# Kernel optimization log

Hardware: AMD Instinct MI355X
Metric: run time of the kernel (lower is better)

Reference implementation:

```python
import jax, jax.numpy as jnp
import numpy as np

N = 100000   # nodes
E = 1600000  # edges
G = 64       # graphs
D = 64       # latent_dim
NF = 128     # num_node_feats
EF = 32      # num_edge_feats
NV = 5000    # num_node_val_feats
LV = 3       # max_lv
EPS = 1e-5


def setup_inputs() -> dict:
    key = jax.random.key(0)
    ks = jax.random.split(key, 16)
    s = 0.05
    return {
        "node_feat": jax.random.normal(ks[0], (N, NF), jnp.float32),
        "edge_feat": jax.random.normal(ks[1], (E, EF), jnp.float32),
        "w_n2l_W": jax.random.normal(ks[2], (NF, D), jnp.float32) * s,
        "w_n2l_b": jnp.zeros((D,), jnp.float32),
        "node_val_embedding": jax.random.normal(ks[3], (NV, D), jnp.float32) * s,
        "w_e2l_W": jax.random.normal(ks[4], (LV + 1, EF, D), jnp.float32) * s,
        "w_e2l_b": jnp.zeros((LV + 1, D), jnp.float32),
        "conv_W": jax.random.normal(ks[5], (LV, D, D), jnp.float32) * s,
        "conv_b": jnp.zeros((LV, D), jnp.float32),
        "l2_W": jax.random.normal(ks[6], (LV, D, D), jnp.float32) * s,
        "l2_b": jnp.zeros((LV, D), jnp.float32),
        "msg_g": jnp.ones((LV + 1, D), jnp.float32),
        "msg_b": jnp.zeros((LV + 1, D), jnp.float32),
        "hid_g": jnp.ones((LV, D), jnp.float32),
        "hid_b": jnp.zeros((LV, D), jnp.float32),
        "out_W": jax.random.normal(ks[7], (D, D), jnp.float32) * s,
        "out_b": jnp.zeros((D,), jnp.float32),
        "edge_from": jax.random.randint(ks[8], (E,), 0, N, jnp.int32),
        "edge_to": jax.random.randint(ks[9], (E,), 0, N, jnp.int32),
        "g_idx": jnp.sort(jax.random.randint(ks[10], (N,), 0, G, jnp.int32)),
        "node_val_idx": jax.random.randint(ks[11], (N,), 0, NV, jnp.int32),
    }


def _bn(x, g, b):
    # BatchNorm1d in training mode: biased batch stats
    m = jnp.mean(x, axis=0)
    v = jnp.mean(jnp.square(x - m), axis=0)
    return (x - m) * jax.lax.rsqrt(v + EPS) * g + b


def reference(node_feat, edge_feat, w_n2l_W, w_n2l_b, node_val_embedding,
              w_e2l_W, w_e2l_b, conv_W, conv_b, l2_W, l2_b,
              msg_g, msg_b, hid_g, hid_b, out_W, out_b,
              edge_from, edge_to, g_idx, node_val_idx):
    act = jax.nn.relu
    # input node transform + sparse node-value embedding (one-hot spmm == gather)
    h = node_feat @ w_n2l_W + w_n2l_b + node_val_embedding[node_val_idx]
    # edge->node pool for level 0
    e0 = edge_feat @ w_e2l_W[0] + w_e2l_b[0]
    h = h + jax.ops.segment_sum(e0, edge_to, num_segments=N)
    h = _bn(act(h), msg_g[0], msg_b[0])
    for lv in range(LV):
        # MessagePassing with add-aggr: gather sources, scatter-add to targets, then Linear
        agg = jax.ops.segment_sum(h[edge_from], edge_to, num_segments=N)
        node_linear = agg @ conv_W[lv] + conv_b[lv]
        e = edge_feat @ w_e2l_W[lv + 1] + w_e2l_b[lv + 1]
        merged = act(node_linear + jax.ops.segment_sum(e, edge_to, num_segments=N))
        merged = _bn(merged, hid_g[lv], hid_b[lv])
        h = _bn(act(merged @ l2_W[lv] + l2_b[lv] + h), msg_g[lv + 1], msg_b[lv + 1])
    # readout: gnn_out='last', readout_agg='max', act_last=True, bn=False
    pooled = jax.ops.segment_max(h, g_idx, num_segments=G)
    return act(pooled @ out_W + out_b)
```

## Files before the change

kernel.cpp:

```cpp
#include <hip/hip_runtime.h>
#include <math.h>

#define NN 100000
#define EE 1600000
#define GG 64
#define DD 64
#define NF 128
#define EF 32
#define LVL 3
#define EPSBN 1e-5f
#define NTILES ((NN + 63) / 64)
#define NBS ((NN + 255) / 256)

typedef unsigned short u16;
typedef unsigned int u32;
typedef short s4v __attribute__((ext_vector_type(4)));
typedef short bf16x8 __attribute__((ext_vector_type(8)));
typedef float f32x4 __attribute__((ext_vector_type(4)));

__device__ __forceinline__ float4 ld4(const float* p) { return *(const float4*)p; }
__device__ __forceinline__ u16 f2b(float f) {
    u32 u = __float_as_uint(f);
    return (u16)((u + 0x7FFFu + ((u >> 16) & 1u)) >> 16);
}
__device__ __forceinline__ float b2f(u16 u) { return __uint_as_float(((u32)u) << 16); }
__device__ __forceinline__ float blo(u32 u) { return __uint_as_float(u << 16); }
__device__ __forceinline__ float bhi(u32 u) { return __uint_as_float(u & 0xFFFF0000u); }

__global__ void khist(const int* __restrict__ to, int* __restrict__ cnt) {
    int e = blockIdx.x * blockDim.x + threadIdx.x;
    if (e < EE) atomicAdd(&cnt[to[e]], 1);
}

__global__ void kbsum(const int* __restrict__ cnt, int* __restrict__ bsum) {
    __shared__ int s[256];
    int t = threadIdx.x;
    int i = blockIdx.x * 256 + t;
    s[t] = (i < NN) ? cnt[i] : 0;
    __syncthreads();
    for (int off = 128; off > 0; off >>= 1) {
        if (t < off) s[t] += s[t + off];
        __syncthreads();
    }
    if (t == 0) bsum[blockIdx.x] = s[0];
}

__global__ void kbscan(const int* __restrict__ bsum, int* __restrict__ boff) {
    __shared__ int s[512];
    int t = threadIdx.x;
    s[t] = (t < NBS) ? bsum[t] : 0;
    __syncthreads();
    for (int off = 1; off < 512; off <<= 1) {
        int v = (t >= off) ? s[t - off] : 0;
        __syncthreads();
        s[t] += v;
        __syncthreads();
    }
    if (t < NBS) boff[t] = (t == 0) ? 0 : s[t - 1];
}

__global__ void kfscan(const int* __restrict__ cnt, const int* __restrict__ boff,
                       int* __restrict__ row_ptr, int* __restrict__ cursor) {
    __shared__ int s[256];
    int t = threadIdx.x;
    int b = blockIdx.x;
    int i = b * 256 + t;
    int v = (i < NN) ? cnt[i] : 0;
    s[t] = v;
    __syncthreads();
    for (int off = 1; off < 256; off <<= 1) {
        int u = (t >= off) ? s[t - off] : 0;
        __syncthreads();
        s[t] += u;
        __syncthreads();
    }
    if (i < NN) {
        int excl = boff[b] + s[t] - v;
        row_ptr[i] = excl;
        cursor[i] = excl;
        if (i == NN - 1) row_ptr[NN] = boff[b] + s[t];
    }
}

__global__ void kreorder(const int* __restrict__ to, const int* __restrict__ from,
                         int* __restrict__ cursor, int2* __restrict__ pair) {
    int e = blockIdx.x * blockDim.x + threadIdx.x;
    if (e < EE) {
        int pos = atomicAdd(&cursor[to[e]], 1);
        pair[pos] = make_int2(e, from[e]);
    }
}

__global__ void kpool(const float* __restrict__ ef, const int* __restrict__ row_ptr,
                      const int2* __restrict__ pair, u16* __restrict__ pooled) {
    int lane = threadIdx.x & 63;
    int wid = threadIdx.x >> 6;
    int w = lane & 31, half = lane >> 5;
    for (int n = blockIdx.x * 4 + wid; n < NN; n += gridDim.x * 4) {
        int e0 = row_ptr[n], e1 = row_ptr[n + 1];
        float acc = 0.f;
        int e = e0 + half;
        for (; e + 2 < e1; e += 4) {
            int i0 = pair[e].x, i1 = pair[e + 2].x;
            float v0 = ef[(size_t)i0 * EF + w];
            float v1 = ef[(size_t)i1 * EF + w];
            acc += v0 + v1;
        }
        if (e < e1) acc += ef[(size_t)pair[e].x * EF + w];
        acc += __shfl_xor(acc, 32);
        if (half == 0) pooled[(size_t)n * EF + w] = f2b(acc);
    }
}

template <int K1, int K2, bool A1BF, bool AAFF, bool EMB, bool BE, bool RESID>
__global__ __launch_bounds__(256) void kgemm_mfma(
    const void* __restrict__ A1v, const u16* __restrict__ A2,
    const float* __restrict__ W1, const float* __restrict__ W2,
    const float* __restrict__ bias, const float* __restrict__ be,
    const int* __restrict__ row_ptr, const float* __restrict__ emb,
    const int* __restrict__ nvi, const u16* __restrict__ resid,
    const float* __restrict__ raff, const float* __restrict__ aaff,
    u16* __restrict__ Xb, float* __restrict__ stats) {
    constexpr int K = K1 + K2;
    constexpr int KP = K + 8;
    __shared__ u16 A_lds[64 * KP];
    __shared__ u16 Wt_lds[64 * KP];
    __shared__ float red[128];

    const int t = threadIdx.x;
    const int lane = t & 63;
    const int wv = t >> 6;
    const int l15 = lane & 15;
    const int lg = lane >> 4;

    for (int idx = t; idx < K * 16; idx += 256) {
        int k = idx >> 4, c4 = (idx & 15) * 4;
        float4 w4 = (k < K1) ? ld4(W1 + (size_t)k * 64 + c4)
                             : ld4(W2 + (size_t)(k - K1) * 64 + c4);
        Wt_lds[(c4 + 0) * KP + k] = f2b(w4.x);
        Wt_lds[(c4 + 1) * KP + k] = f2b(w4.y);
        Wt_lds[(c4 + 2) * KP + k] = f2b(w4.z);
        Wt_lds[(c4 + 3) * KP + k] = f2b(w4.w);
    }
    if (t < 128) red[t] = 0.f;

    float bias_c[4], be_c[4], rsc_c[4], rsh_c[4];
#pragma unroll
    for (int n = 0; n < 4; n++) {
        int ch = 16 * n + l15;
        bias_c[n] = bias[ch];
        be_c[n] = BE ? be[ch] : 0.f;
        rsc_c[n] = RESID ? raff[ch] : 0.f;
        rsh_c[n] = RESID ? raff[64 + ch] : 0.f;
    }

    for (int tile = blockIdx.x; tile < NTILES; tile += gridDim.x) {
        int nb = tile * 64;
        __syncthreads();
        if (A1BF) {
            const u16* A1b = (const u16*)A1v;
            for (int idx = t; idx < 64 * (K1 / 4); idx += 256) {
                int node = idx / (K1 / 4), kq = (idx % (K1 / 4)) * 4;
                int gn = nb + node;
                s4v v = {0, 0, 0, 0};
                if (gn < NN) {
                    v = *(const s4v*)(A1b + (size_t)gn * K1 + kq);
                    if (AAFF) {
#pragma unroll
                        for (int i = 0; i < 4; i++) {
                            float f = b2f((u16)v[i]) * aaff[kq + i] + aaff[64 + kq + i];
                            v[i] = (short)f2b(f);
                        }
                    }
                }
                *(s4v*)&A_lds[node * KP + kq] = v;
            }
        } else {
            const float* A1f = (const float*)A1v;
            for (int idx = t; idx < 64 * (K1 / 4); idx += 256) {
                int node = idx / (K1 / 4), kq = (idx % (K1 / 4)) * 4;
                int gn = nb + node;
                s4v v = {0, 0, 0, 0};
                if (gn < NN) {
                    float4 a = ld4(A1f + (size_t)gn * K1 + kq);
                    v[0] = (short)f2b(a.x); v[1] = (short)f2b(a.y);
                    v[2] = (short)f2b(a.z); v[3] = (short)f2b(a.w);
                }
                *(s4v*)&A_lds[node * KP + kq] = v;
            }
        }
        if (K2 > 0) {
            for (int idx = t; idx < 64 * (K2 / 4); idx += 256) {
                int node = idx / (K2 / 4), kq = (idx % (K2 / 4)) * 4;
                int gn = nb + node;
                s4v v = {0, 0, 0, 0};
                if (gn < NN) v = *(const s4v*)(A2 + (size_t)gn * K2 + kq);
                *(s4v*)&A_lds[node * KP + K1 + kq] = v;
            }
        }
        __syncthreads();

        f32x4 acc[4];
#pragma unroll
        for (int n = 0; n < 4; n++) acc[n] = (f32x4){0.f, 0.f, 0.f, 0.f};
        const int arow = 16 * wv + l15;
#pragma unroll
        for (int kk = 0; kk < K; kk += 32) {
            s4v alo = *(const s4v*)&A_lds[arow * KP + kk + lg * 4];
            s4v ahi = *(const s4v*)&A_lds[arow * KP + kk + lg * 4 + 16];
            bf16x8 a = __builtin_shufflevector(alo, ahi, 0, 1, 2, 3, 4, 5, 6, 7);
#pragma unroll
            for (int n = 0; n < 4; n++) {
                s4v wlo = *(const s4v*)&Wt_lds[(16 * n + l15) * KP + kk + lg * 4];
                s4v whi = *(const s4v*)&Wt_lds[(16 * n + l15) * KP + kk + lg * 4 + 16];
                bf16x8 b = __builtin_shufflevector(wlo, whi, 0, 1, 2, 3, 4, 5, 6, 7);
                acc[n] = __builtin_amdgcn_mfma_f32_16x16x32_bf16(a, b, acc[n], 0, 0, 0);
            }
        }

        float ss[4] = {0, 0, 0, 0}, sq2[4] = {0, 0, 0, 0};
#pragma unroll
        for (int r = 0; r < 4; r++) {
            int node = nb + 16 * wv + lg * 4 + r;
            if (node < NN) {
                float deg = BE ? (float)(row_ptr[node + 1] - row_ptr[node]) : 0.f;
                int nv = EMB ? nvi[node] : 0;
#pragma unroll
                for (int n = 0; n < 4; n++) {
                    int ch = 16 * n + l15;
                    float v = acc[n][r] + bias_c[n];
                    if (BE) v += deg * be_c[n];
                    if (EMB) v += emb[(size_t)nv * 64 + ch];
                    if (RESID) v += b2f(resid[(size_t)node * 64 + ch]) * rsc_c[n] + rsh_c[n];
                    v = fmaxf(v, 0.f);
                    Xb[(size_t)node * 64 + ch] = f2b(v);
                    ss[n] += v;
                    sq2[n] += v * v;
                }
            }
        }
#pragma unroll
        for (int n = 0; n < 4; n++) {
            float a = ss[n];
            a += __shfl_xor(a, 16);
            a += __shfl_xor(a, 32);
            float b = sq2[n];
            b += __shfl_xor(b, 16);
            b += __shfl_xor(b, 32);
            if (lg == 0) {
                atomicAdd(&red[16 * n + l15], a);
                atomicAdd(&red[64 + 16 * n + l15], b);
            }
        }
    }
    __syncthreads();
    if (t < 128) atomicAdd(&stats[t], red[t]);
}

__global__ void kfin(float* __restrict__ stats, const float* __restrict__ g,
                     const float* __restrict__ b, int slot) {
    int t = threadIdx.x;
    float mean = stats[t] * (1.0f / NN);
    float var = stats[64 + t] * (1.0f / NN) - mean * mean;
    float rstd = rsqrtf(fmaxf(var, 0.f) + EPSBN);
    float sc = g[t] * rstd;
    float* slotp = stats + 128 + slot * 128;
    slotp[t] = sc;
    slotp[64 + t] = b[t] - mean * sc;
    stats[t] = 0.f;
    stats[64 + t] = 0.f;
}

__global__ void kmsg_bf(const u32* __restrict__ h2, const int* __restrict__ row_ptr,
                        const int2* __restrict__ pair, const float* __restrict__ aff,
                        u32* __restrict__ agg) {
    int lane = threadIdx.x & 63;
    int wid = threadIdx.x >> 6;
    int w = lane & 31, half = lane >> 5;
    float sc0 = aff[2 * w], sc1 = aff[2 * w + 1];
    float sh0 = aff[64 + 2 * w], sh1 = aff[64 + 2 * w + 1];
    for (int n = blockIdx.x * 4 + wid; n < NN; n += gridDim.x * 4) {
        int e0 = row_ptr[n], e1 = row_ptr[n + 1];
        float a0 = 0.f, a1 = 0.f;
        int e = e0;
        for (; e + 16 <= e1; e += 16) {
            int s0 = pair[e + half].y, s1 = pair[e + 2 + half].y;
            int s2 = pair[e + 4 + half].y, s3 = pair[e + 6 + half].y;
            int s4 = pair[e + 8 + half].y, s5 = pair[e + 10 + half].y;
            int s6 = pair[e + 12 + half].y, s7 = pair[e + 14 + half].y;
            u32 u0 = h2[(size_t)s0 * 32 + w];
            u32 u1 = h2[(size_t)s1 * 32 + w];
            u32 u2 = h2[(size_t)s2 * 32 + w];
            u32 u3 = h2[(size_t)s3 * 32 + w];
            u32 u4 = h2[(size_t)s4 * 32 + w];
            u32 u5 = h2[(size_t)s5 * 32 + w];
            u32 u6 = h2[(size_t)s6 * 32 + w];
            u32 u7 = h2[(size_t)s7 * 32 + w];
            a0 += ((blo(u0) + blo(u1)) + (blo(u2) + blo(u3))) +
                  ((blo(u4) + blo(u5)) + (blo(u6) + blo(u7)));
            a1 += ((bhi(u0) + bhi(u1)) + (bhi(u2) + bhi(u3))) +
                  ((bhi(u4) + bhi(u5)) + (bhi(u6) + bhi(u7)));
        }
        for (; e + 8 <= e1; e += 8) {
            int s0 = pair[e + half].y, s1 = pair[e + 2 + half].y;
            int s2 = pair[e + 4 + half].y, s3 = pair[e + 6 + half].y;
            u32 u0 = h2[(size_t)s0 * 32 + w];
            u32 u1 = h2[(size_t)s1 * 32 + w];
            u32 u2 = h2[(size_t)s2 * 32 + w];
            u32 u3 = h2[(size_t)s3 * 32 + w];
            a0 += (blo(u0) + blo(u1)) + (blo(u2) + blo(u3));
            a1 += (bhi(u0) + bhi(u1)) + (bhi(u2) + bhi(u3));
        }
        for (; e < e1; e += 2) {
            if (e + half < e1) {
                u32 u = h2[(size_t)pair[e + half].y * 32 + w];
                a0 += blo(u);
                a1 += bhi(u);
            }
        }
        a0 += __shfl_xor(a0, 32);
        a1 += __shfl_xor(a1, 32);
        if (half == 0) {
            float deg = (float)(e1 - e0);
            u16 o0 = f2b(sc0 * a0 + deg * sh0);
            u16 o1 = f2b(sc1 * a1 + deg * sh1);
            agg[(size_t)n * 32 + w] = (u32)o0 | ((u32)o1 << 16);
        }
    }
}

__device__ __forceinline__ unsigned fenc(float f) {
    unsigned u = __float_as_uint(f);
    return (u >> 31) ? ~u : (u | 0x80000000u);
}
__device__ __forceinline__ float fdec(unsigned k) {
    return (k >> 31) ? __uint_as_float(k ^ 0x80000000u) : __uint_as_float(~k);
}

__global__ void kinitpk(unsigned* __restrict__ pk) {
    int i = blockIdx.x * blockDim.x + threadIdx.x;
    if (i < GG * DD) pk[i] = 0x007FFFFFu;
}

__global__ void kread(const u16* __restrict__ h2, const int* __restrict__ gidx,
                      const float* __restrict__ aff, unsigned* __restrict__ pk) {
    int lane = threadIdx.x & 63;
    int wid = threadIdx.x >> 6;
    float sc = aff[lane], sh = aff[64 + lane];
    int gw = blockIdx.x * 4 + wid;
    int nw = gridDim.x * 4;
    int chunk = (NN + nw - 1) / nw;
    int lo = gw * chunk, hi = min(lo + chunk, NN);
    if (lo >= hi) return;
    int cur = gidx[lo];
    float acc = -INFINITY;
    for (int n = lo; n < hi; n++) {
        int g = gidx[n];
        if (g != cur) {
            atomicMax(&pk[cur * DD + lane], fenc(acc));
            cur = g;
            acc = -INFINITY;
        }
        acc = fmaxf(acc, b2f(h2[(size_t)n * 64 + lane]) * sc + sh);
    }
    atomicMax(&pk[cur * DD + lane], fenc(acc));
}

__global__ void kout(const unsigned* __restrict__ pk, const float* __restrict__ W,
                     const float* __restrict__ b, float* __restrict__ out) {
    int t = blockIdx.x * blockDim.x + threadIdx.x;
    int g = t >> 6, d = t & 63;
    float acc = b[d];
    for (int k = 0; k < DD; k++) {
        float p = fdec(pk[g * DD + k]);
        acc += p * W[k * DD + d];
    }
    out[t] = fmaxf(acc, 0.f);
}

extern "C" void kernel_launch(void* const* d_in, const int* in_sizes, int n_in,
                              void* d_out, int out_size, void* d_ws, size_t ws_size,
                              hipStream_t stream) {
    const float* node_feat = (const float*)d_in[0];
    const float* edge_feat = (const float*)d_in[1];
    const float* w_n2l_W = (const float*)d_in[2];
    const float* w_n2l_b = (const float*)d_in[3];
    const float* nve = (const float*)d_in[4];
    const float* w_e2l_W = (const float*)d_in[5];
    const float* w_e2l_b = (const float*)d_in[6];
    const float* conv_W = (const float*)d_in[7];
    const float* conv_b = (const float*)d_in[8];
    const float* l2_W = (const float*)d_in[9];
    const float* l2_b = (const float*)d_in[10];
    const float* msg_g = (const float*)d_in[11];
    const float* msg_b = (const float*)d_in[12];
    const float* hid_g = (const float*)d_in[13];
    const float* hid_b = (const float*)d_in[14];
    const float* out_W = (const float*)d_in[15];
    const float* out_b = (const float*)d_in[16];
    const int* edge_from = (const int*)d_in[17];
    const int* edge_to = (const int*)d_in[18];
    const int* g_idx = (const int*)d_in[19];
    const int* nvi = (const int*)d_in[20];
    float* out = (float*)d_out;

    char* ws = (char*)d_ws;
    size_t off = 0;
    auto alloc = [&](size_t bytes) -> void* {
        void* p = ws + off;
        off += (bytes + 255) / 256 * 256;
        return p;
    };
    int* cnt = (int*)alloc((size_t)NN * 4);
    int* row_ptr = (int*)alloc((size_t)(NN + 1) * 4);
    int* cursor = (int*)alloc((size_t)NN * 4);
    int2* pair = (int2*)alloc((size_t)EE * 8);
    u16* pooled_ef = (u16*)alloc((size_t)NN * EF * 2);
    u16* h2a = (u16*)alloc((size_t)NN * DD * 2);
    u16* h2b = (u16*)alloc((size_t)NN * DD * 2);
    u16* agg_bf = (u16*)alloc((size_t)NN * DD * 2);
    u16* mb_bf = (u16*)alloc((size_t)NN * DD * 2);
    float* stats = (float*)alloc(1024 * 4);
    unsigned* pk = (unsigned*)alloc((size_t)GG * DD * 4);
    int* bsum = (int*)alloc((size_t)NBS * 4);
    int* boff = (int*)alloc((size_t)512 * 4);
    (void)ws_size; (void)n_in; (void)in_sizes; (void)out_size;

    hipMemsetAsync(cnt, 0, (size_t)NN * 4, stream);
    hipMemsetAsync(stats, 0, 1024 * 4, stream);
    kinitpk<<<16, 256, 0, stream>>>(pk);

    khist<<<(EE + 255) / 256, 256, 0, stream>>>(edge_to, cnt);
    kbsum<<<NBS, 256, 0, stream>>>(cnt, bsum);
    kbscan<<<1, 512, 0, stream>>>(bsum, boff);
    kfscan<<<NBS, 256, 0, stream>>>(cnt, boff, row_ptr, cursor);
    kreorder<<<(EE + 255) / 256, 256, 0, stream>>>(edge_to, edge_from, cursor, pair);
    kpool<<<2048, 256, 0, stream>>>(edge_feat, row_ptr, pair, pooled_ef);

    const int GB = 782;

    kgemm_mfma<NF, EF, false, false, true, true, false>
        <<<GB, 256, 0, stream>>>(node_feat, pooled_ef, w_n2l_W, w_e2l_W,
                                 w_n2l_b, w_e2l_b, row_ptr, nve, nvi,
                                 nullptr, nullptr, nullptr, h2a, stats);
    kfin<<<1, 64, 0, stream>>>(stats, msg_g, msg_b, 0);

    u16* hcur = h2a;
    u16* hnext = h2b;
    for (int lv = 0; lv < LVL; lv++) {
        kmsg_bf<<<2048, 256, 0, stream>>>((const u32*)hcur, row_ptr, pair,
                                          stats + 128 + lv * 128, (u32*)agg_bf);
        kgemm_mfma<DD, EF, true, false, false, true, false>
            <<<GB, 256, 0, stream>>>(agg_bf, pooled_ef, conv_W + lv * DD * DD,
                                     w_e2l_W + (size_t)(lv + 1) * EF * DD,
                                     conv_b + lv * DD,
                                     w_e2l_b + (size_t)(lv + 1) * DD, row_ptr,
                                     nullptr, nullptr, nullptr, nullptr, nullptr,
                                     mb_bf, stats);
        kfin<<<1, 64, 0, stream>>>(stats, hid_g + lv * DD, hid_b + lv * DD, 4 + lv);
        kgemm_mfma<DD, 0, true, true, false, false, true>
            <<<GB, 256, 0, stream>>>(mb_bf, nullptr, l2_W + lv * DD * DD, nullptr,
                                     l2_b + lv * DD, nullptr, row_ptr, nullptr,
                                     nullptr, hcur, stats + 128 + lv * 128,
                                     stats + 128 + (4 + lv) * 128, hnext, stats);
        kfin<<<1, 64, 0, stream>>>(stats, msg_g + (lv + 1) * DD, msg_b + (lv + 1) * DD,
                                   lv + 1);
        u16* tmp = hcur; hcur = hnext; hnext = tmp;
    }

    kread<<<1024, 256, 0, stream>>>(hcur, g_idx, stats + 128 + LVL * 128, pk);
    kout<<<GG, 64, 0, stream>>>(pk, out_W, out_b, out);
}
```

Baseline: 710.1 us.

## Replace global-atomic CSR build with two-pass bucketed counting sort

Builds the destination-sorted edge list with a two-level bucket sort: a coarse histogram over 256-node buckets in shared memory, a scan, a scatter into bucket-contiguous temp storage, then a per-bucket fine sort in LDS that emits row_ptr and pairs. This replaces per-edge global atomics on 100k counters and scattered writes with mostly shared-memory atomics and more local writes. The kpool loop is also unrolled to four gathers per iteration. The cost is an extra temp buffer and an extra pass over the edges. Edge order within a node becomes nondeterministic, as it already was.

```diff
diff --git a/kernel.cpp b/kernel.cpp
--- a/kernel.cpp
+++ b/kernel.cpp
@@ -10,7 +10,7 @@
 #define LVL 3
 #define EPSBN 1e-5f
 #define NTILES ((NN + 63) / 64)
-#define NBS ((NN + 255) / 256)
+#define NBKT 391
 
 typedef unsigned short u16;
 typedef unsigned int u32;
@@ -27,28 +27,23 @@
 __device__ __forceinline__ float blo(u32 u) { return __uint_as_float(u << 16); }
 __device__ __forceinline__ float bhi(u32 u) { return __uint_as_float(u & 0xFFFF0000u); }
 
-__global__ void khist(const int* __restrict__ to, int* __restrict__ cnt) {
-    int e = blockIdx.x * blockDim.x + threadIdx.x;
-    if (e < EE) atomicAdd(&cnt[to[e]], 1);
-}
-
-__global__ void kbsum(const int* __restrict__ cnt, int* __restrict__ bsum) {
-    __shared__ int s[256];
-    int t = threadIdx.x;
-    int i = blockIdx.x * 256 + t;
-    s[t] = (i < NN) ? cnt[i] : 0;
-    __syncthreads();
-    for (int off = 128; off > 0; off >>= 1) {
-        if (t < off) s[t] += s[t + off];
-        __syncthreads();
-    }
-    if (t == 0) bsum[blockIdx.x] = s[0];
-}
-
-__global__ void kbscan(const int* __restrict__ bsum, int* __restrict__ boff) {
+
+__global__ void k1b(const int* __restrict__ to, int* __restrict__ bhist) {
+    __shared__ int h[NBKT];
+    for (int i = threadIdx.x; i < NBKT; i += 256) h[i] = 0;
+    __syncthreads();
+    for (int e = blockIdx.x * 256 + threadIdx.x; e < EE; e += 256 * gridDim.x)
+        atomicAdd(&h[to[e] >> 8], 1);
+    __syncthreads();
+    for (int i = threadIdx.x; i < NBKT; i += 256)
+        if (h[i]) atomicAdd(&bhist[i], h[i]);
+}
+
+__global__ void k1c(const int* __restrict__ bhist, int* __restrict__ bbase,
+                    int* __restrict__ gcur) {
     __shared__ int s[512];
     int t = threadIdx.x;
-    s[t] = (t < NBS) ? bsum[t] : 0;
+    s[t] = (t < NBKT) ? bhist[t] : 0;
     __syncthreads();
     for (int off = 1; off < 512; off <<= 1) {
         int v = (t >= off) ? s[t - off] : 0;
@@ -56,38 +51,61 @@
         s[t] += v;
         __syncthreads();
     }
-    if (t < NBS) boff[t] = (t == 0) ? 0 : s[t - 1];
-}
-
-__global__ void kfscan(const int* __restrict__ cnt, const int* __restrict__ boff,
-                       int* __restrict__ row_ptr, int* __restrict__ cursor) {
+    if (t < NBKT) {
+        int base = t ? s[t - 1] : 0;
+        bbase[t] = base;
+        gcur[t] = base;
+    }
+    if (t == NBKT - 1) bbase[NBKT] = s[t];
+}
+
+__global__ void k1d(const int* __restrict__ to, const int* __restrict__ from,
+                    int* __restrict__ gcur, int2* __restrict__ tmp) {
+    __shared__ int h[NBKT];
+    __shared__ int cur[NBKT];
+    for (int i = threadIdx.x; i < NBKT; i += 256) h[i] = 0;
+    __syncthreads();
+    for (int e = blockIdx.x * 256 + threadIdx.x; e < EE; e += 256 * gridDim.x)
+        atomicAdd(&h[to[e] >> 8], 1);
+    __syncthreads();
+    for (int i = threadIdx.x; i < NBKT; i += 256)
+        cur[i] = h[i] ? atomicAdd(&gcur[i], h[i]) : 0;
+    __syncthreads();
+    for (int e = blockIdx.x * 256 + threadIdx.x; e < EE; e += 256 * gridDim.x) {
+        int tt = to[e];
+        int b = tt >> 8;
+        int pos = atomicAdd(&cur[b], 1);
+        tmp[pos] = make_int2(from[e] | ((tt & 255) << 17), e);
+    }
+}
+
+__global__ void kp2(const int2* __restrict__ tmp, const int* __restrict__ bbase,
+                    int* __restrict__ row_ptr, int2* __restrict__ pair) {
     __shared__ int s[256];
-    int t = threadIdx.x;
-    int b = blockIdx.x;
-    int i = b * 256 + t;
-    int v = (i < NN) ? cnt[i] : 0;
-    s[t] = v;
-    __syncthreads();
+    __shared__ int cur[256];
+    int b = blockIdx.x, t = threadIdx.x;
+    int e0 = bbase[b], e1 = bbase[b + 1];
+    s[t] = 0;
+    __syncthreads();
+    for (int e = e0 + t; e < e1; e += 256) atomicAdd(&s[(tmp[e].x >> 17) & 255], 1);
+    __syncthreads();
+    int v = s[t];
     for (int off = 1; off < 256; off <<= 1) {
         int u = (t >= off) ? s[t - off] : 0;
         __syncthreads();
         s[t] += u;
         __syncthreads();
     }
-    if (i < NN) {
-        int excl = boff[b] + s[t] - v;
-        row_ptr[i] = excl;
-        cursor[i] = excl;
-        if (i == NN - 1) row_ptr[NN] = boff[b] + s[t];
-    }
-}
-
-__global__ void kreorder(const int* __restrict__ to, const int* __restrict__ from,
-                         int* __restrict__ cursor, int2* __restrict__ pair) {
-    int e = blockIdx.x * blockDim.x + threadIdx.x;
-    if (e < EE) {
-        int pos = atomicAdd(&cursor[to[e]], 1);
-        pair[pos] = make_int2(e, from[e]);
+    int excl = e0 + s[t] - v;
+    cur[t] = excl;
+    int n = b * 256 + t;
+    if (n < NN) row_ptr[n] = excl;
+    if (b == NBKT - 1 && t == 0) row_ptr[NN] = e1;
+    __syncthreads();
+    for (int e = e0 + t; e < e1; e += 256) {
+        int2 w = tmp[e];
+        int pos = atomicAdd(&cur[(w.x >> 17) & 255], 1);
+        pair[pos] = make_int2(w.y, w.x & 0x1FFFF);
     }
 }
 
@@ -100,13 +118,16 @@
         int e0 = row_ptr[n], e1 = row_ptr[n + 1];
         float acc = 0.f;
         int e = e0 + half;
-        for (; e + 2 < e1; e += 4) {
+        for (; e + 6 < e1; e += 8) {
             int i0 = pair[e].x, i1 = pair[e + 2].x;
+            int i2 = pair[e + 4].x, i3 = pair[e + 6].x;
             float v0 = ef[(size_t)i0 * EF + w];
             float v1 = ef[(size_t)i1 * EF + w];
-            acc += v0 + v1;
-        }
-        if (e < e1) acc += ef[(size_t)pair[e].x * EF + w];
+            float v2 = ef[(size_t)i2 * EF + w];
+            float v3 = ef[(size_t)i3 * EF + w];
+            acc += (v0 + v1) + (v2 + v3);
+        }
+        for (; e < e1; e += 2) acc += ef[(size_t)pair[e].x * EF + w];
         acc += __shfl_xor(acc, 32);
         if (half == 0) pooled[(size_t)n * EF + w] = f2b(acc);
     }
@@ -411,10 +432,9 @@
         off += (bytes + 255) / 256 * 256;
         return p;
     };
-    int* cnt = (int*)alloc((size_t)NN * 4);
     int* row_ptr = (int*)alloc((size_t)(NN + 1) * 4);
-    int* cursor = (int*)alloc((size_t)NN * 4);
     int2* pair = (int2*)alloc((size_t)EE * 8);
+    int2* tmp = (int2*)alloc((size_t)EE * 8);
     u16* pooled_ef = (u16*)alloc((size_t)NN * EF * 2);
     u16* h2a = (u16*)alloc((size_t)NN * DD * 2);
     u16* h2b = (u16*)alloc((size_t)NN * DD * 2);
@@ -422,19 +442,19 @@
     u16* mb_bf = (u16*)alloc((size_t)NN * DD * 2);
     float* stats = (float*)alloc(1024 * 4);
     unsigned* pk = (unsigned*)alloc((size_t)GG * DD * 4);
-    int* bsum = (int*)alloc((size_t)NBS * 4);
-    int* boff = (int*)alloc((size_t)512 * 4);
+    int* bhist = (int*)alloc((size_t)NBKT * 4);
+    int* bbase = (int*)alloc((size_t)(NBKT + 1) * 4);
+    int* gcur = (int*)alloc((size_t)NBKT * 4);
     (void)ws_size; (void)n_in; (void)in_sizes; (void)out_size;
 
-    hipMemsetAsync(cnt, 0, (size_t)NN * 4, stream);
+    hipMemsetAsync(bhist, 0, (size_t)NBKT * 4, stream);
     hipMemsetAsync(stats, 0, 1024 * 4, stream);
     kinitpk<<<16, 256, 0, stream>>>(pk);
 
-    khist<<<(EE + 255) / 256, 256, 0, stream>>>(edge_to, cnt);
-    kbsum<<<NBS, 256, 0, stream>>>(cnt, bsum);
-    kbscan<<<1, 512, 0, stream>>>(bsum, boff);
-    kfscan<<<NBS, 256, 0, stream>>>(cnt, boff, row_ptr, cursor);
-    kreorder<<<(EE + 255) / 256, 256, 0, stream>>>(edge_to, edge_from, cursor, pair);
+    k1b<<<256, 256, 0, stream>>>(edge_to, bhist);
+    k1c<<<1, 512, 0, stream>>>(bhist, bbase, gcur);
+    k1d<<<256, 256, 0, stream>>>(edge_to, edge_from, gcur, tmp);
+    kp2<<<NBKT, 256, 0, stream>>>(tmp, bbase, row_ptr, pair);
     kpool<<<2048, 256, 0, stream>>>(edge_feat, row_ptr, pair, pooled_ef);
 
     const int GB = 782;
@@ -465,7 +485,7 @@
                                      stats + 128 + (4 + lv) * 128, hnext, stats);
         kfin<<<1, 64, 0, stream>>>(stats, msg_g + (lv + 1) * DD, msg_b + (lv + 1) * DD,
                                    lv + 1);
-        u16* tmp = hcur; hcur = hnext; hnext = tmp;
+        u16* tmp2 = hcur; hcur = hnext; hnext = tmp2;
     }
 
     kread<<<1024, 256, 0, stream>>>(hcur, g_idx, stats + 128 + LVL * 128, pk);
```

After: 584.5 us. -17.7%, faster.
